# Performance work log

Hardware: AMD Instinct MI355X
Metric: run time of the kernel (lower is better)

The kernel has to match this reference:

```python
import jax, jax.numpy as jnp
import numpy as np

N = 50000      # nodes
E = 800000     # edges (before self-loops)
IN_CH = 5
HID = 32
HEADS = 4
NEG_SLOPE = 0.2  # PyG GATConv default


def _gat_layer(x, src, dst, W, att_src, att_dst, bias, concat):
    """PyG GATConv (eval mode). W: [F_in, H*C], att_*: [H, C], bias matches output."""
    H, C = att_src.shape
    h = (x @ W).reshape(-1, H, C)                       # [N, H, C]
    a_src = jnp.sum(h * att_src, axis=-1)               # [N, H]
    a_dst = jnp.sum(h * att_dst, axis=-1)               # [N, H]
    e = jax.nn.leaky_relu(a_src[src] + a_dst[dst], negative_slope=NEG_SLOPE)  # [E', H]
    m = jax.ops.segment_max(e, dst, num_segments=N)     # stable softmax per dst segment
    ex = jnp.exp(e - m[dst])
    denom = jax.ops.segment_sum(ex, dst, num_segments=N)
    alpha = ex / denom[dst]                             # [E', H]
    out = jax.ops.segment_sum(alpha[:, :, None] * h[src], dst, num_segments=N)  # [N, H, C]
    out = out.reshape(N, H * C) if concat else out.mean(axis=1)
    return out + bias


def setup_inputs() -> dict:
    key = jax.random.key(0)
    ks = jax.random.split(key, 14)
    g = lambda k, shape, s=0.1: (jax.random.normal(k, shape, jnp.float32) * s)
    return {
        "x": jax.random.normal(ks[0], (N, IN_CH), jnp.float32),
        "edge_index": jax.random.randint(ks[1], (2, E), 0, N, jnp.int32),
        "W1": g(ks[2], (IN_CH, HEADS * HID)),
        "att_src1": g(ks[3], (HEADS, HID)),
        "att_dst1": g(ks[4], (HEADS, HID)),
        "b1": jnp.zeros((HEADS * HID,), jnp.float32),
        "W2": g(ks[5], (HEADS * HID, HID)),
        "att_src2": g(ks[6], (1, HID)),
        "att_dst2": g(ks[7], (1, HID)),
        "b2": jnp.zeros((HID,), jnp.float32),
        "Wc1": g(ks[8], (HID, 16)),
        "bc1": jnp.zeros((16,), jnp.float32),
        "Wc2": g(ks[9], (16, 1)),
        "bc2": jnp.zeros((1,), jnp.float32),
    }


def reference(x, edge_index, W1, att_src1, att_dst1, b1, W2, att_src2, att_dst2, b2, Wc1, bc1, Wc2, bc2):
    # add self loops (PyG GATConv default add_self_loops=True)
    loops = jnp.arange(N, dtype=edge_index.dtype)
    src = jnp.concatenate([edge_index[0], loops])
    dst = jnp.concatenate([edge_index[1], loops])
    # dropout layers are identity in eval mode
    h = jax.nn.elu(_gat_layer(x, src, dst, W1, att_src1, att_dst1, b1, concat=True))
    h = jax.nn.elu(_gat_layer(h, src, dst, W2, att_src2, att_dst2, b2, concat=False))
    h = jax.nn.relu(h @ Wc1 + bc1)
    out = (h @ Wc2 + bc2)[:, 0]   # squeeze(-1) -> [N]
    return out
```

## Files before the change

### kernel.cpp

```cpp
#include <hip/hip_runtime.h>
#include <hip/hip_fp16.h>

#define NEG_SLOPE 0.2f
#define BSHIFT 6
#define SCATB 256

__device__ __forceinline__ float elu1(float v) { return v > 0.f ? v : expm1f(v); }
__device__ __forceinline__ float lrelu(float v) { return v > 0.f ? v : NEG_SLOPE * v; }


__global__ __launch_bounds__(256) void k_cnt(
    const int* __restrict__ ei, int E, int ET, int chunk,
    int* __restrict__ Cmat, int nbuck) {
    __shared__ int hist[784];
    for (int i = threadIdx.x; i < nbuck; i += 256) hist[i] = 0;
    __syncthreads();
    int k = blockIdx.x;
    int e0 = k * chunk, e1 = min(e0 + chunk, ET);
    for (int e = e0 + threadIdx.x; e < e1; e += 256) {
        int d = (e < E) ? ei[E + e] : e - E;
        atomicAdd(&hist[d >> BSHIFT], 1);
    }
    __syncthreads();
    for (int i = threadIdx.x; i < nbuck; i += 256)
        Cmat[i * SCATB + k] = hist[i];
}

__global__ __launch_bounds__(256) void k_scan1(
    const int* __restrict__ Cmat, int* __restrict__ blkoff, int* __restrict__ bsum, int M) {
    __shared__ int ws4[4], wsoff[4];
    int i = blockIdx.x * 256 + threadIdx.x;
    int lane = threadIdx.x & 63, w = threadIdx.x >> 6;
    int v = (i < M) ? Cmat[i] : 0;
    int sc = v;
#pragma unroll
    for (int m = 1; m < 64; m <<= 1) {
        int t = __shfl_up(sc, m, 64);
        if (lane >= m) sc += t;
    }
    if (lane == 63) ws4[w] = sc;
    __syncthreads();
    if (threadIdx.x == 0) {
        int r = 0;
#pragma unroll
        for (int j = 0; j < 4; ++j) { wsoff[j] = r; r += ws4[j]; }
        bsum[blockIdx.x] = r;
    }
    __syncthreads();
    if (i < M) blkoff[i + 1] = sc + wsoff[w];
}

__global__ __launch_bounds__(1024) void k_scan2(int* __restrict__ bsum, int nb) {
    __shared__ int wsum[16];
    int i = threadIdx.x, lane = i & 63, w = i >> 6;
    int v = (i < nb) ? bsum[i] : 0, sc = v;
#pragma unroll
    for (int m = 1; m < 64; m <<= 1) {
        int t = __shfl_up(sc, m, 64);
        if (lane >= m) sc += t;
    }
    if (lane == 63) wsum[w] = sc;
    __syncthreads();
    if (w == 0 && lane < 16) {
        int s2 = wsum[lane];
#pragma unroll
        for (int m = 1; m < 16; m <<= 1) {
            int t = __shfl_up(s2, m, 16);
            if (lane >= m) s2 += t;
        }
        wsum[lane] = s2;
    }
    __syncthreads();
    int carry = (w == 0) ? 0 : wsum[w - 1];
    if (i < nb) bsum[i] = carry + sc;
}

__global__ __launch_bounds__(256) void k_scan3(
    int* __restrict__ blkoff, const int* __restrict__ bsum,
    int* __restrict__ off, int M, int N, int ET) {
    int i = blockIdx.x * 256 + threadIdx.x;
    if (i == 0) { blkoff[0] = 0; off[N] = ET; }
    if (i >= M) return;
    if (blockIdx.x > 0) blkoff[i + 1] += bsum[blockIdx.x - 1];
}

__global__ __launch_bounds__(256) void k_scat(
    const int* __restrict__ ei, int E, int ET, int chunk,
    const int* __restrict__ blkoff, unsigned* __restrict__ pairs, int nbuck) {
    __shared__ int cur[784];
    int k = blockIdx.x;
    for (int i = threadIdx.x; i < nbuck; i += 256)
        cur[i] = blkoff[i * SCATB + k];
    __syncthreads();
    int e0 = k * chunk, e1 = min(e0 + chunk, ET);
    for (int e = e0 + threadIdx.x; e < e1; e += 256) {
        int s, d;
        if (e < E) { s = ei[e]; d = ei[E + e]; } else { s = d = e - E; }
        int p = atomicAdd(&cur[d >> BSHIFT], 1);
        pairs[p] = (unsigned)s | ((unsigned)(d & 63) << 16);
    }
}

__global__ __launch_bounds__(256) void k_sortB(
    const unsigned* __restrict__ pairs, const int* __restrict__ blkoff,
    int* __restrict__ off, int* __restrict__ csr_src, int N, int ET, int nbuck) {
    __shared__ int hist[64], cur[64];
    int b = blockIdx.x;
    int base = blkoff[b * SCATB];
    int end  = (b + 1 < nbuck) ? blkoff[(b + 1) * SCATB] : ET;
    int cnt = end - base;
    int dstBase = b << BSHIFT;
    if (threadIdx.x < 64) hist[threadIdx.x] = 0;
    __syncthreads();
    for (int i = threadIdx.x; i < cnt; i += 256)
        atomicAdd(&hist[pairs[base + i] >> 16], 1);
    __syncthreads();
    if (threadIdx.x < 64) {
        int v = hist[threadIdx.x], sc = v;
#pragma unroll
        for (int m = 1; m < 64; m <<= 1) {
            int t = __shfl_up(sc, m, 64);
            if (threadIdx.x >= m) sc += t;
        }
        int ex = sc - v;
        cur[threadIdx.x] = ex;
        int d = dstBase + threadIdx.x;
        if (d < N) off[d] = base + ex;
    }
    __syncthreads();
    for (int i = threadIdx.x; i < cnt; i += 256) {
        unsigned pr = pairs[base + i];
        int r = atomicAdd(&cur[pr >> 16], 1);
        csr_src[base + r] = (int)(pr & 0xFFFFu);
    }
}


__global__ __launch_bounds__(256) void k_attn1(
    const float* __restrict__ x, const float* __restrict__ W1,
    const float* __restrict__ att_s, const float* __restrict__ att_d,
    float* __restrict__ rec, int N) {
    __shared__ float Ps[5][4], Pd[5][4];
    if (threadIdx.x < 40) {
        int pair = threadIdx.x & 1, idx = threadIdx.x >> 1;
        int k = idx >> 2, h = idx & 3;
        const float* att = pair ? att_d : att_s;
        float r = 0.f;
#pragma unroll
        for (int c = 0; c < 32; ++c) r = fmaf(W1[k * 128 + h * 32 + c], att[h * 32 + c], r);
        if (pair) Pd[k][h] = r; else Ps[k][h] = r;
    }
    __syncthreads();
    int n = blockIdx.x * 256 + threadIdx.x;
    if (n >= N) return;
    float xv[5];
#pragma unroll
    for (int k = 0; k < 5; ++k) xv[k] = x[(size_t)n * 5 + k];
    float s0 = 0, s1 = 0, s2 = 0, s3 = 0, d0 = 0, d1 = 0, d2 = 0, d3 = 0;
#pragma unroll
    for (int k = 0; k < 5; ++k) {
        s0 = fmaf(xv[k], Ps[k][0], s0); s1 = fmaf(xv[k], Ps[k][1], s1);
        s2 = fmaf(xv[k], Ps[k][2], s2); s3 = fmaf(xv[k], Ps[k][3], s3);
        d0 = fmaf(xv[k], Pd[k][0], d0); d1 = fmaf(xv[k], Pd[k][1], d1);
        d2 = fmaf(xv[k], Pd[k][2], d2); d3 = fmaf(xv[k], Pd[k][3], d3);
    }
    float* r = rec + (size_t)n * 16;
    *(float4*)(r)     = make_float4(s0, s1, s2, s3);
    *(float4*)(r + 4) = make_float4(xv[0], xv[1], xv[2], xv[3]);
    r[8] = xv[4];
    *(float4*)(r + 12) = make_float4(d0, d1, d2, d3);
}

__global__ __launch_bounds__(256) void k_agg1(
    const int* __restrict__ off, const int* __restrict__ csr_src,
    const float* __restrict__ rec, const float* __restrict__ W1,
    const float* __restrict__ b1, __half* __restrict__ out1h, int N) {
    __shared__ float Wl[5 * 128];
    __shared__ float b1l[128];
    for (int i = threadIdx.x; i < 5 * 128; i += 256) Wl[i] = W1[i];
    if (threadIdx.x < 128) b1l[threadIdx.x] = b1[threadIdx.x];
    __syncthreads();
    int g = (blockIdx.x * 256 + threadIdx.x) >> 4;
    int lane = threadIdx.x & 15;
    if (g >= N) return;
    int p0 = off[g], p1 = off[g + 1];
    float4 ad = *(const float4*)(rec + (size_t)g * 16 + 12);
    float den0 = 0, den1 = 0, den2 = 0, den3 = 0;
    float acc[4][5] = {};
    for (int p = p0 + lane; p < p1; p += 16) {
        int s = csr_src[p];
        const float* r = rec + (size_t)s * 16;
        float4 as  = *(const float4*)r;
        float4 x03 = *(const float4*)(r + 4);
        float  x4  = r[8];
        float v0 = __expf(lrelu(as.x + ad.x));
        float v1 = __expf(lrelu(as.y + ad.y));
        float v2 = __expf(lrelu(as.z + ad.z));
        float v3 = __expf(lrelu(as.w + ad.w));
        den0 += v0; den1 += v1; den2 += v2; den3 += v3;
        float xk[5] = {x03.x, x03.y, x03.z, x03.w, x4};
#pragma unroll
        for (int k = 0; k < 5; ++k) {
            acc[0][k] = fmaf(v0, xk[k], acc[0][k]);
            acc[1][k] = fmaf(v1, xk[k], acc[1][k]);
            acc[2][k] = fmaf(v2, xk[k], acc[2][k]);
            acc[3][k] = fmaf(v3, xk[k], acc[3][k]);
        }
    }
#pragma unroll
    for (int m = 8; m; m >>= 1) {
        den0 += __shfl_xor(den0, m, 16); den1 += __shfl_xor(den1, m, 16);
        den2 += __shfl_xor(den2, m, 16); den3 += __shfl_xor(den3, m, 16);
#pragma unroll
        for (int h = 0; h < 4; ++h)
#pragma unroll
            for (int k = 0; k < 5; ++k) acc[h][k] += __shfl_xor(acc[h][k], m, 16);
    }
    int c0 = lane * 8;
    int h = lane >> 2;
    float dh = (h == 0) ? den0 : (h == 1) ? den1 : (h == 2) ? den2 : den3;
    float ih = 1.f / dh;
    float ag[5];
#pragma unroll
    for (int k = 0; k < 5; ++k) ag[k] = acc[h][k] * ih;
    __half2 ph[4];
#pragma unroll
    for (int j = 0; j < 4; ++j) {
        float oa, ob;
        {
            int c = c0 + 2 * j;
            float rr = b1l[c];
#pragma unroll
            for (int k = 0; k < 5; ++k) rr = fmaf(ag[k], Wl[k * 128 + c], rr);
            oa = elu1(rr);
            rr = b1l[c + 1];
#pragma unroll
            for (int k = 0; k < 5; ++k) rr = fmaf(ag[k], Wl[k * 128 + c + 1], rr);
            ob = elu1(rr);
        }
        ph[j] = __floats2half2_rn(oa, ob);
    }
    *(float4*)(out1h + (size_t)g * 128 + c0) = *(float4*)ph;
}


__global__ __launch_bounds__(256) void k_feat2(
    const __half* __restrict__ out1h, const float* __restrict__ W2,
    const float* __restrict__ att_s, const float* __restrict__ att_d,
    __half* __restrict__ h2h, float* __restrict__ a_s, float* __restrict__ a_d, int N) {
    __shared__ float Wl[128 * 32];
    for (int i = threadIdx.x; i < 128 * 32; i += 256) Wl[i] = W2[i];
    __syncthreads();
    int t = blockIdx.x * 256 + threadIdx.x;
    int n = t >> 5, c = t & 31;
    if (n >= N) return;
    const float4* hr4 = (const float4*)(out1h + (size_t)n * 128);
    float acc = 0.f;
#pragma unroll
    for (int k4 = 0; k4 < 16; ++k4) {
        float4 q = hr4[k4];
        const __half2* hp = (const __half2*)&q;
#pragma unroll
        for (int m = 0; m < 4; ++m) {
            float2 f = __half22float2(hp[m]);
            acc = fmaf(f.x, Wl[(k4 * 8 + 2 * m) * 32 + c], acc);
            acc = fmaf(f.y, Wl[(k4 * 8 + 2 * m + 1) * 32 + c], acc);
        }
    }
    h2h[(size_t)n * 32 + c] = __float2half_rn(acc);
    float as = acc * att_s[c], ad = acc * att_d[c];
#pragma unroll
    for (int m = 16; m; m >>= 1) {
        as += __shfl_xor(as, m, 32);
        ad += __shfl_xor(ad, m, 32);
    }
    if (c == 0) { a_s[n] = as; a_d[n] = ad; }
}

__global__ __launch_bounds__(256) void k_agg2h(
    const int* __restrict__ off, const int* __restrict__ csr_src,
    const float* __restrict__ a_s, const float* __restrict__ a_d,
    const __half* __restrict__ h2h, const float* __restrict__ b2,
    const float* __restrict__ Wc1, const float* __restrict__ bc1,
    const float* __restrict__ Wc2, const float* __restrict__ bc2,
    float* __restrict__ out, int N) {
    __shared__ float Wl[512];
    __shared__ float b2l[32], b1l[16], w2l[16];
    for (int i = threadIdx.x; i < 512; i += 256) Wl[i] = Wc1[i];
    if (threadIdx.x < 32) b2l[threadIdx.x] = b2[threadIdx.x];
    if (threadIdx.x < 16) {
        b1l[threadIdx.x] = bc1[threadIdx.x];
        w2l[threadIdx.x] = Wc2[threadIdx.x];
    }
    __syncthreads();
    int g = (blockIdx.x * 256 + threadIdx.x) >> 5;
    int lane = threadIdx.x & 31;
    if (g >= N) return;
    int p0 = off[g], p1 = off[g + 1];
    float ad = a_d[g];
    float acc = 0.f, den = 0.f;
    for (int base = p0; base < p1; base += 32) {
        int rem = p1 - base;
        int s = g;
        float w = 0.f;
        if (lane < rem) {
            s = csr_src[base + lane];
            w = __expf(lrelu(a_s[s] + ad));
        }
        den += w;
        int cnt = min(rem, 32);
        int rc = (cnt + 7) & ~7;
        for (int j = 0; j < rc; j += 8) {
#pragma unroll
            for (int jj = 0; jj < 8; ++jj) {
                int   sj = __shfl(s, j + jj, 32);
                float wj = __shfl(w, j + jj, 32);
                float hv = __half2float(h2h[(size_t)sj * 32 + lane]);
                acc = fmaf(wj, hv, acc);
            }
        }
    }
#pragma unroll
    for (int m = 16; m; m >>= 1) den += __shfl_xor(den, m, 32);
    float z = elu1(fmaf(acc, 1.f / den, b2l[lane]));
    float y = b1l[lane & 15];
#pragma unroll
    for (int c = 0; c < 32; ++c) {
        float zc = __shfl(z, c, 32);
        y = fmaf(zc, Wl[c * 16 + (lane & 15)], y);
    }
    y = fmaxf(y, 0.f);
    float t = (lane < 16) ? y * w2l[lane] : 0.f;
#pragma unroll
    for (int m = 8; m; m >>= 1) t += __shfl_xor(t, m, 32);
    if (lane == 0) out[g] = t + bc2[0];
}

extern "C" void kernel_launch(void* const* d_in, const int* in_sizes, int n_in,
                              void* d_out, int out_size, void* d_ws, size_t ws_size,
                              hipStream_t stream) {
    const float* x   = (const float*)d_in[0];
    const int*   ei  = (const int*)d_in[1];
    const float* W1  = (const float*)d_in[2];
    const float* as1 = (const float*)d_in[3];
    const float* ad1 = (const float*)d_in[4];
    const float* b1  = (const float*)d_in[5];
    const float* W2  = (const float*)d_in[6];
    const float* as2 = (const float*)d_in[7];
    const float* ad2 = (const float*)d_in[8];
    const float* b2  = (const float*)d_in[9];
    const float* Wc1 = (const float*)d_in[10];
    const float* bc1 = (const float*)d_in[11];
    const float* Wc2 = (const float*)d_in[12];
    const float* bc2 = (const float*)d_in[13];
    float* out = (float*)d_out;

    const int N = out_size;
    const int E = in_sizes[1] / 2;
    const int ET = E + N;
    const int nbuck = (N + 63) >> BSHIFT;
    const int M = nbuck * SCATB;
    const int chunk = (ET + SCATB - 1) / SCATB;

    float*    ws    = (float*)d_ws;
    __half*   out1h = (__half*)ws;
    __half*   h2h   = (__half*)(ws + (size_t)N * 64);
    float*    rec   = ws + (size_t)N * 80;
    float*    a_s2  = rec  + (size_t)N * 16;
    float*    a_d2  = a_s2 + N;
    int*      off   = (int*)(a_d2 + N);
    int*      csr_src = off + (N + 2);
    int*      Cmat  = csr_src + ET;
    int*      blkoff = Cmat + M;
    int*      bsum  = blkoff + (M + 2);
    unsigned* pairs = (unsigned*)(bsum + 1024);

    auto cdiv = [](long long a, long long b) { return (int)((a + b - 1) / b); };
    const int B = 256;
    const int NB2 = cdiv(M, B);

    k_cnt<<<SCATB, B, 0, stream>>>(ei, E, ET, chunk, Cmat, nbuck);
    k_scan1<<<NB2, B, 0, stream>>>(Cmat, blkoff, bsum, M);
    k_scan2<<<1, 1024, 0, stream>>>(bsum, NB2);
    k_scan3<<<NB2, B, 0, stream>>>(blkoff, bsum, off, M, N, ET);
    k_scat<<<SCATB, B, 0, stream>>>(ei, E, ET, chunk, blkoff, pairs, nbuck);
    k_sortB<<<nbuck, B, 0, stream>>>(pairs, blkoff, off, csr_src, N, ET, nbuck);

    k_attn1<<<cdiv(N, B), B, 0, stream>>>(x, W1, as1, ad1, rec, N);
    k_agg1<<<cdiv((long long)N * 16, B), B, 0, stream>>>(off, csr_src, rec, W1, b1, out1h, N);

    k_feat2<<<cdiv((long long)N * 32, B), B, 0, stream>>>(out1h, W2, as2, ad2, h2h, a_s2, a_d2, N);
    k_agg2h<<<cdiv((long long)N * 32, B), B, 0, stream>>>(off, csr_src, a_s2, a_d2, h2h, b2,
                                                          Wc1, bc1, Wc2, bc2, out, N);
}
```

Before: 120.3 us.

## Fuse attention precompute into count kernel and eliminate scan3 pass

```diff
diff --git a/kernel.cpp b/kernel.cpp
--- a/kernel.cpp
+++ b/kernel.cpp
@@ -8,22 +8,66 @@
 __device__ __forceinline__ float elu1(float v) { return v > 0.f ? v : expm1f(v); }
 __device__ __forceinline__ float lrelu(float v) { return v > 0.f ? v : NEG_SLOPE * v; }
 
-
-__global__ __launch_bounds__(256) void k_cnt(
+__device__ __forceinline__ int ge_off(const int* __restrict__ blkoff,
+                                      const int* __restrict__ bsum2, int j) {
+    if (j == 0) return 0;
+    int b = (j - 1) >> 8;
+    int v = blkoff[j];
+    if (b >= 1) v += bsum2[b - 1];
+    return v;
+}
+
+
+__global__ __launch_bounds__(256) void k_cnt_attn(
     const int* __restrict__ ei, int E, int ET, int chunk,
-    int* __restrict__ Cmat, int nbuck) {
+    int* __restrict__ Cmat, int nbuck,
+    const float* __restrict__ x, const float* __restrict__ W1,
+    const float* __restrict__ att_s, const float* __restrict__ att_d,
+    float* __restrict__ rec, int N) {
     __shared__ int hist[784];
-    for (int i = threadIdx.x; i < nbuck; i += 256) hist[i] = 0;
-    __syncthreads();
-    int k = blockIdx.x;
-    int e0 = k * chunk, e1 = min(e0 + chunk, ET);
-    for (int e = e0 + threadIdx.x; e < e1; e += 256) {
-        int d = (e < E) ? ei[E + e] : e - E;
-        atomicAdd(&hist[d >> BSHIFT], 1);
-    }
-    __syncthreads();
-    for (int i = threadIdx.x; i < nbuck; i += 256)
-        Cmat[i * SCATB + k] = hist[i];
+    __shared__ float Ps[5][4], Pd[5][4];
+    if (blockIdx.x < SCATB) {
+        for (int i = threadIdx.x; i < nbuck; i += 256) hist[i] = 0;
+        __syncthreads();
+        int k = blockIdx.x;
+        int e0 = k * chunk, e1 = min(e0 + chunk, ET);
+        for (int e = e0 + threadIdx.x; e < e1; e += 256) {
+            int d = (e < E) ? ei[E + e] : e - E;
+            atomicAdd(&hist[d >> BSHIFT], 1);
+        }
+        __syncthreads();
+        for (int i = threadIdx.x; i < nbuck; i += 256)
+            Cmat[i * SCATB + k] = hist[i];
+    } else {
+        if (threadIdx.x < 40) {
+            int pair = threadIdx.x & 1, idx = threadIdx.x >> 1;
+            int k = idx >> 2, h = idx & 3;
+            const float* att = pair ? att_d : att_s;
+            float r = 0.f;
+#pragma unroll
+            for (int c = 0; c < 32; ++c) r = fmaf(W1[k * 128 + h * 32 + c], att[h * 32 + c], r);
+            if (pair) Pd[k][h] = r; else Ps[k][h] = r;
+        }
+        __syncthreads();
+        int n = (blockIdx.x - SCATB) * 256 + threadIdx.x;
+        if (n >= N) return;
+        float xv[5];
+#pragma unroll
+        for (int k = 0; k < 5; ++k) xv[k] = x[(size_t)n * 5 + k];
+        float s0 = 0, s1 = 0, s2 = 0, s3 = 0, d0 = 0, d1 = 0, d2 = 0, d3 = 0;
+#pragma unroll
+        for (int k = 0; k < 5; ++k) {
+            s0 = fmaf(xv[k], Ps[k][0], s0); s1 = fmaf(xv[k], Ps[k][1], s1);
+            s2 = fmaf(xv[k], Ps[k][2], s2); s3 = fmaf(xv[k], Ps[k][3], s3);
+            d0 = fmaf(xv[k], Pd[k][0], d0); d1 = fmaf(xv[k], Pd[k][1], d1);
+            d2 = fmaf(xv[k], Pd[k][2], d2); d3 = fmaf(xv[k], Pd[k][3], d3);
+        }
+        float* r = rec + (size_t)n * 16;
+        *(float4*)(r)      = make_float4(s0, s1, s2, s3);
+        *(float4*)(r + 4)  = make_float4(xv[0], xv[1], xv[2], xv[3]);
+        r[8] = xv[4];
+        *(float4*)(r + 12) = make_float4(d0, d1, d2, d3);
+    }
 }
 
 __global__ __launch_bounds__(256) void k_scan1(
@@ -50,9 +94,11 @@
     if (i < M) blkoff[i + 1] = sc + wsoff[w];
 }
 
-__global__ __launch_bounds__(1024) void k_scan2(int* __restrict__ bsum, int nb) {
+__global__ __launch_bounds__(1024) void k_scan2(
+    int* __restrict__ bsum, int nb, int* __restrict__ off, int N, int ET) {
     __shared__ int wsum[16];
     int i = threadIdx.x, lane = i & 63, w = i >> 6;
+    if (i == 0) off[N] = ET;
     int v = (i < nb) ? bsum[i] : 0, sc = v;
 #pragma unroll
     for (int m = 1; m < 64; m <<= 1) {
@@ -75,22 +121,14 @@
     if (i < nb) bsum[i] = carry + sc;
 }
 
-__global__ __launch_bounds__(256) void k_scan3(
-    int* __restrict__ blkoff, const int* __restrict__ bsum,
-    int* __restrict__ off, int M, int N, int ET) {
-    int i = blockIdx.x * 256 + threadIdx.x;
-    if (i == 0) { blkoff[0] = 0; off[N] = ET; }
-    if (i >= M) return;
-    if (blockIdx.x > 0) blkoff[i + 1] += bsum[blockIdx.x - 1];
-}
-
 __global__ __launch_bounds__(256) void k_scat(
     const int* __restrict__ ei, int E, int ET, int chunk,
-    const int* __restrict__ blkoff, unsigned* __restrict__ pairs, int nbuck) {
+    const int* __restrict__ blkoff, const int* __restrict__ bsum2,
+    unsigned* __restrict__ pairs, int nbuck) {
     __shared__ int cur[784];
     int k = blockIdx.x;
     for (int i = threadIdx.x; i < nbuck; i += 256)
-        cur[i] = blkoff[i * SCATB + k];
+        cur[i] = ge_off(blkoff, bsum2, i * SCATB + k);
     __syncthreads();
     int e0 = k * chunk, e1 = min(e0 + chunk, ET);
     for (int e = e0 + threadIdx.x; e < e1; e += 256) {
@@ -103,17 +141,23 @@
 
 __global__ __launch_bounds__(256) void k_sortB(
     const unsigned* __restrict__ pairs, const int* __restrict__ blkoff,
-    int* __restrict__ off, int* __restrict__ csr_src, int N, int ET, int nbuck) {
+    const int* __restrict__ bsum2, int* __restrict__ off,
+    int* __restrict__ csr_src, int N, int ET, int nbuck) {
     __shared__ int hist[64], cur[64];
+    __shared__ unsigned pl[1536];
     int b = blockIdx.x;
-    int base = blkoff[b * SCATB];
-    int end  = (b + 1 < nbuck) ? blkoff[(b + 1) * SCATB] : ET;
+    int base = ge_off(blkoff, bsum2, b * SCATB);
+    int end  = (b + 1 < nbuck) ? ge_off(blkoff, bsum2, (b + 1) * SCATB) : ET;
     int cnt = end - base;
+    int stg = min(cnt, 1536);
     int dstBase = b << BSHIFT;
     if (threadIdx.x < 64) hist[threadIdx.x] = 0;
-    __syncthreads();
-    for (int i = threadIdx.x; i < cnt; i += 256)
-        atomicAdd(&hist[pairs[base + i] >> 16], 1);
+    for (int i = threadIdx.x; i < stg; i += 256) pl[i] = pairs[base + i];
+    __syncthreads();
+    for (int i = threadIdx.x; i < cnt; i += 256) {
+        unsigned pr = (i < stg) ? pl[i] : pairs[base + i];
+        atomicAdd(&hist[pr >> 16], 1);
+    }
     __syncthreads();
     if (threadIdx.x < 64) {
         int v = hist[threadIdx.x], sc = v;
@@ -129,47 +173,12 @@
     }
     __syncthreads();
     for (int i = threadIdx.x; i < cnt; i += 256) {
-        unsigned pr = pairs[base + i];
+        unsigned pr = (i < stg) ? pl[i] : pairs[base + i];
         int r = atomicAdd(&cur[pr >> 16], 1);
         csr_src[base + r] = (int)(pr & 0xFFFFu);
     }
 }
 
-
-__global__ __launch_bounds__(256) void k_attn1(
-    const float* __restrict__ x, const float* __restrict__ W1,
-    const float* __restrict__ att_s, const float* __restrict__ att_d,
-    float* __restrict__ rec, int N) {
-    __shared__ float Ps[5][4], Pd[5][4];
-    if (threadIdx.x < 40) {
-        int pair = threadIdx.x & 1, idx = threadIdx.x >> 1;
-        int k = idx >> 2, h = idx & 3;
-        const float* att = pair ? att_d : att_s;
-        float r = 0.f;
-#pragma unroll
-        for (int c = 0; c < 32; ++c) r = fmaf(W1[k * 128 + h * 32 + c], att[h * 32 + c], r);
-        if (pair) Pd[k][h] = r; else Ps[k][h] = r;
-    }
-    __syncthreads();
-    int n = blockIdx.x * 256 + threadIdx.x;
-    if (n >= N) return;
-    float xv[5];
-#pragma unroll
-    for (int k = 0; k < 5; ++k) xv[k] = x[(size_t)n * 5 + k];
-    float s0 = 0, s1 = 0, s2 = 0, s3 = 0, d0 = 0, d1 = 0, d2 = 0, d3 = 0;
-#pragma unroll
-    for (int k = 0; k < 5; ++k) {
-        s0 = fmaf(xv[k], Ps[k][0], s0); s1 = fmaf(xv[k], Ps[k][1], s1);
-        s2 = fmaf(xv[k], Ps[k][2], s2); s3 = fmaf(xv[k], Ps[k][3], s3);
-        d0 = fmaf(xv[k], Pd[k][0], d0); d1 = fmaf(xv[k], Pd[k][1], d1);
-        d2 = fmaf(xv[k], Pd[k][2], d2); d3 = fmaf(xv[k], Pd[k][3], d3);
-    }
-    float* r = rec + (size_t)n * 16;
-    *(float4*)(r)     = make_float4(s0, s1, s2, s3);
-    *(float4*)(r + 4) = make_float4(xv[0], xv[1], xv[2], xv[3]);
-    r[8] = xv[4];
-    *(float4*)(r + 12) = make_float4(d0, d1, d2, d3);
-}
 
 __global__ __launch_bounds__(256) void k_agg1(
     const int* __restrict__ off, const int* __restrict__ csr_src,
@@ -226,18 +235,15 @@
     __half2 ph[4];
 #pragma unroll
     for (int j = 0; j < 4; ++j) {
-        float oa, ob;
-        {
-            int c = c0 + 2 * j;
-            float rr = b1l[c];
-#pragma unroll
-            for (int k = 0; k < 5; ++k) rr = fmaf(ag[k], Wl[k * 128 + c], rr);
-            oa = elu1(rr);
-            rr = b1l[c + 1];
-#pragma unroll
-            for (int k = 0; k < 5; ++k) rr = fmaf(ag[k], Wl[k * 128 + c + 1], rr);
-            ob = elu1(rr);
-        }
+        int c = c0 + 2 * j;
+        float rr = b1l[c];
+#pragma unroll
+        for (int k = 0; k < 5; ++k) rr = fmaf(ag[k], Wl[k * 128 + c], rr);
+        float oa = elu1(rr);
+        rr = b1l[c + 1];
+#pragma unroll
+        for (int k = 0; k < 5; ++k) rr = fmaf(ag[k], Wl[k * 128 + c + 1], rr);
+        float ob = elu1(rr);
         ph[j] = __floats2half2_rn(oa, ob);
     }
     *(float4*)(out1h + (size_t)g * 128 + c0) = *(float4*)ph;
@@ -378,15 +384,15 @@
     auto cdiv = [](long long a, long long b) { return (int)((a + b - 1) / b); };
     const int B = 256;
     const int NB2 = cdiv(M, B);
-
-    k_cnt<<<SCATB, B, 0, stream>>>(ei, E, ET, chunk, Cmat, nbuck);
+    const int nAttn = cdiv(N, B);
+
+    k_cnt_attn<<<SCATB + nAttn, B, 0, stream>>>(ei, E, ET, chunk, Cmat, nbuck,
+                                                x, W1, as1, ad1, rec, N);
     k_scan1<<<NB2, B, 0, stream>>>(Cmat, blkoff, bsum, M);
-    k_scan2<<<1, 1024, 0, stream>>>(bsum, NB2);
-    k_scan3<<<NB2, B, 0, stream>>>(blkoff, bsum, off, M, N, ET);
-    k_scat<<<SCATB, B, 0, stream>>>(ei, E, ET, chunk, blkoff, pairs, nbuck);
-    k_sortB<<<nbuck, B, 0, stream>>>(pairs, blkoff, off, csr_src, N, ET, nbuck);
-
-    k_attn1<<<cdiv(N, B), B, 0, stream>>>(x, W1, as1, ad1, rec, N);
+    k_scan2<<<1, 1024, 0, stream>>>(bsum, NB2, off, N, ET);
+    k_scat<<<SCATB, B, 0, stream>>>(ei, E, ET, chunk, blkoff, bsum, pairs, nbuck);
+    k_sortB<<<nbuck, B, 0, stream>>>(pairs, blkoff, bsum, off, csr_src, N, ET, nbuck);
+
     k_agg1<<<cdiv((long long)N * 16, B), B, 0, stream>>>(off, csr_src, rec, W1, b1, out1h, N);
 
     k_feat2<<<cdiv((long long)N * 32, B), B, 0, stream>>>(out1h, W2, as2, ad2, h2h, a_s2, a_d2, N);
```

New measurement: 117.6 us. 2.2% less time.
